# Kernel tuning notes

Measured on AMD Instinct MI355X. Metric: run time of the kernel, lower is better.

## Reference

```python
import jax, jax.numpy as jnp
import numpy as np

SAMPLE_SIZE = 4096  # deterministic mode: first SAMPLE_SIZE flattened pixels
EPS_STD = 1e-8
EPS_PDF = 1e-10


def _std(v):
    # torch.std is unbiased (ddof=1)
    return jnp.std(v, ddof=1)


def _adaptive_sigma(v):
    # sigma=None path: 0.2 * std, clamped to [0.001, 1.0]
    return jnp.clip(_std(v) * 0.2, 0.001, 1.0)


def _normalize(v):
    return (v - jnp.mean(v)) / (_std(v) + EPS_STD)


def _marginal_pdf(values, sigma):
    vn = _normalize(values)                      # [N]
    resid = vn[None, :] - vn[:, None]            # [N, N]
    kernel = jnp.exp(-0.5 * (resid / sigma) ** 2)
    pdf = jnp.mean(kernel, axis=1)               # [N]
    return pdf / (jnp.sum(pdf) + EPS_PDF)


def _joint_pdf(v1, v2, s1, s2):
    vn1 = _normalize(v1)
    vn2 = _normalize(v2)
    r1 = vn1[None, :] - vn1[:, None]             # [N, N]
    r2 = vn2[None, :] - vn2[:, None]             # [N, N]
    kernel = jnp.exp(-0.5 * (r1 / s1) ** 2) * jnp.exp(-0.5 * (r2 / s2) ** 2)
    pdf = jnp.mean(kernel, axis=1)
    return pdf / (jnp.sum(pdf) + EPS_PDF)


def _mi_kde(img1, img2):
    x = img1.reshape(-1)[:SAMPLE_SIZE]
    y = img2.reshape(-1)[:SAMPLE_SIZE]
    s1 = _adaptive_sigma(x)
    s2 = _adaptive_sigma(y)
    p1 = _marginal_pdf(x, s1)
    p2 = _marginal_pdf(y, s2)
    pj = _joint_pdf(x, y, s1, s2)
    ratio = (pj + EPS_PDF) / (p1 * p2 + EPS_PDF)
    log_ratio = jnp.log(jnp.clip(ratio, 1e-10, 1e10))
    return jnp.sum(pj * log_ratio)


def setup_inputs() -> dict:
    key = jax.random.key(0)
    k1, k2, k3 = jax.random.split(key, 3)
    shape = (2, 1, 128, 128)  # [B, C, H, W] images in [0, 1]
    return {
        "fused_img": jax.random.uniform(k1, shape, dtype=jnp.float32),
        "source_img1": jax.random.uniform(k2, shape, dtype=jnp.float32),
        "source_img2": jax.random.uniform(k3, shape, dtype=jnp.float32),
    }


def reference(fused_img, source_img1, source_img2):
    B = fused_img.shape[0]
    total = jnp.float32(0.0)
    for b in range(B):  # small fixed batch loop, matches original
        total = total + _mi_kde(fused_img[b], source_img1[b]) \
                      + _mi_kde(fused_img[b], source_img2[b])
    return -(total / B)
```

## Files before the change

### kernel.cpp

```cpp
#include <hip/hip_runtime.h>

#define N 4096
#define NBIN 1024
#define LOG2E 1.4426950408889634f

__device__ __forceinline__ float fast_exp2(float x) {
#if __has_builtin(__builtin_amdgcn_exp2f)
    return __builtin_amdgcn_exp2f(x);
#else
    return exp2f(x);
#endif
}

__device__ float block_reduce_sum(float v) {
    __shared__ float red[16];
    int lane = threadIdx.x & 63;
    int wid = threadIdx.x >> 6;
    #pragma unroll
    for (int off = 32; off; off >>= 1) v += __shfl_down(v, off, 64);
    if (lane == 0) red[wid] = v;
    __syncthreads();
    if (threadIdx.x == 0) {
        int nw = (int)(blockDim.x >> 6);
        float s = red[0];
        for (int w = 1; w < nw; ++w) s += red[w];
        red[0] = s;
    }
    __syncthreads();
    float r = red[0];
    __syncthreads();
    return r;
}

__device__ float4 block_reduce_stats(float s, float sq, float mn, float mx) {
    __shared__ float4 red4[16];
    int lane = threadIdx.x & 63;
    int wid = threadIdx.x >> 6;
    #pragma unroll
    for (int off = 32; off; off >>= 1) {
        s  += __shfl_down(s, off, 64);
        sq += __shfl_down(sq, off, 64);
        mn  = fminf(mn, __shfl_down(mn, off, 64));
        mx  = fmaxf(mx, __shfl_down(mx, off, 64));
    }
    if (lane == 0) red4[wid] = make_float4(s, sq, mn, mx);
    __syncthreads();
    if (threadIdx.x == 0) {
        float4 r = red4[0];
        #pragma unroll
        for (int w = 1; w < 16; ++w) {
            float4 q = red4[w];
            r.x += q.x; r.y += q.y;
            r.z = fminf(r.z, q.z); r.w = fmaxf(r.w, q.w);
        }
        red4[0] = r;
    }
    __syncthreads();
    float4 r = red4[0];
    __syncthreads();
    return r;
}

__global__ void __launch_bounds__(1024)
k_prep(const float* __restrict__ fused,
       const float* __restrict__ s1,
       const float* __restrict__ s2,
       float2* __restrict__ xa,
       float2* __restrict__ ma,
       float* __restrict__ par,
       float* __restrict__ hcnt,
       float* __restrict__ hmu,
       unsigned int* __restrict__ counter) {
    __shared__ unsigned int cnt[NBIN];
    __shared__ int qs[NBIN];
    int vec = blockIdx.x;
    int b = vec / 3, k = vec % 3;
    const float* src = (k == 0 ? fused : (k == 1 ? s1 : s2)) + b * 16384;
    int tid = threadIdx.x;

    if (vec == 0 && tid == 0) *counter = 0u;
    cnt[tid] = 0u; qs[tid] = 0;

    float v[4];
    float s = 0.f, sq = 0.f, mn = 1e30f, mx = -1e30f;
    #pragma unroll
    for (int t = 0; t < 4; ++t) {
        v[t] = src[tid + t * 1024];
        s += v[t]; sq = fmaf(v[t], v[t], sq);
        mn = fminf(mn, v[t]); mx = fmaxf(mx, v[t]);
    }
    float4 r = block_reduce_stats(s, sq, mn, mx);
    float mean = r.x * (1.0f / 4096.0f);
    float tssq = r.y - 4096.0f * mean * mean;
    float stdv = sqrtf(fmaxf(tssq, 0.f) / 4095.0f);
    float sigma = fminf(fmaxf(0.2f * stdv, 0.001f), 1.0f);
    float inv = 1.0f / (stdv + 1e-8f);
    float c1 = -0.5f * LOG2E / (sigma * sigma);
    float xmin = (r.z - mean) * inv;
    float xmax = (r.w - mean) * inv;
    float range = fmaxf(xmax - xmin, 1e-6f);
    float inv_bw = (float)NBIN / range;
    float binw = range * (1.0f / NBIN);

    float2* xav = xa + (size_t)vec * N;
    float2* mav = ma + (size_t)vec * N;
    __syncthreads();
    #pragma unroll
    for (int t = 0; t < 4; ++t) {
        int i = tid + t * 1024;
        float x = (v[t] - mean) * inv;
        float a = c1 * x * x;
        xav[i] = make_float2(x, a);
        mav[i] = make_float2(-2.0f * c1 * x, a);
        float rel = x - xmin;
        int bb = min(NBIN - 1, max(0, (int)(rel * inv_bw)));
        atomicAdd(&cnt[bb], 1u);
        atomicAdd(&qs[bb], (int)rintf(rel * 16384.0f));
    }
    __syncthreads();
    {
        unsigned int c = cnt[tid];
        hcnt[vec * NBIN + tid] = (float)c;
        float mu = c ? xmin + ((float)qs[tid] / (float)c) * (1.0f / 16384.0f)
                     : xmin + (tid + 0.5f) * binw;
        hmu[vec * NBIN + tid] = mu;
    }
    if (tid == 0) {
        par[vec * 8 + 0] = xmin;
        par[vec * 8 + 1] = inv_bw;
        par[vec * 8 + 2] = binw;
        par[vec * 8 + 3] = c1;
    }
}

__global__ void __launch_bounds__(256, 8)
k_main(const float2* __restrict__ xa,
       const float2* __restrict__ ma,
       const float* __restrict__ par,
       const float* __restrict__ hcnt,
       const float* __restrict__ hmu,
       float* __restrict__ marg,
       float* __restrict__ msum_part,
       float* __restrict__ part, int js) {
    __shared__ float4 sj[128];
    __shared__ float shc[NBIN];
    __shared__ float shm[NBIN];
    const int nib = 4;
    int bid = blockIdx.x;
    int tid = threadIdx.x;

    if (bid < 96) {
        int vec = bid >> 4, ic = bid & 15;
        int i = ic * 256 + tid;
        const float* P = par + vec * 8;
        float xmin = P[0], inv_bw = P[1], c1 = P[3];
        const float* hc = hcnt + vec * NBIN;
        const float* hm = hmu + vec * NBIN;
        #pragma unroll
        for (int u = 0; u < 4; ++u) {
            shc[tid + u * 256] = hc[tid + u * 256];
            shm[tid + u * 256] = hm[tid + u * 256];
        }
        __syncthreads();
        float xi = xa[(size_t)vec * N + i].x;
        float R = sqrtf(45.0f / fabsf(c1));
        int b0 = max(0, (int)((xi - R - xmin) * inv_bw));
        int b1 = min(NBIN - 1, (int)((xi + R - xmin) * inv_bw) + 1);
        float acc = 0.f;
        #pragma unroll 4
        for (int bb = b0; bb <= b1; ++bb) {
            float d = xi - shm[bb];
            acc += shc[bb] * fast_exp2(c1 * d * d);
        }
        float raw = acc * (1.0f / N);
        marg[(size_t)vec * N + i] = raw;
        float tot = block_reduce_sum(raw);
        if (tid == 0) msum_part[bid] = tot;
        return;
    }

    int bid2 = bid - 96;
    int tt = bid2 / (nib * js);
    int rem = bid2 % (nib * js);
    int ib = rem / js, jsp = rem % js;
    int b = tt >> 1, pr = tt & 1;
    int vx = b * 3, vy = b * 3 + 1 + pr;
    int jlen = N / js;
    int j0 = jsp * jlen;
    int ibase = ib * 1024 + tid;

    const float2* xav = xa + (size_t)vx * N;
    const float2* yav = xa + (size_t)vy * N;
    const float2* mxv = ma + (size_t)vx * N;
    const float2* myv = ma + (size_t)vy * N;

    float mx[4], my[4], C[4];
    #pragma unroll
    for (int u = 0; u < 4; ++u) {
        float2 qx = mxv[ibase + u * 256];
        float2 qy = myv[ibase + u * 256];
        mx[u] = qx.x; my[u] = qy.x; C[u] = qx.y + qy.y;
    }
    float acc[4] = {0.f, 0.f, 0.f, 0.f};

    for (int jt = 0; jt < jlen; jt += 128) {
        int cnt = min(128, jlen - jt);
        __syncthreads();
        if (tid < cnt) {
            float2 xq = xav[j0 + jt + tid];
            float2 yq = yav[j0 + jt + tid];
            sj[tid] = make_float4(xq.x, yq.x, xq.y + yq.y, 0.f);
        }
        __syncthreads();
        #pragma unroll 2
        for (int j = 0; j < cnt; j += 2) {
            float4 q0 = sj[j];
            float4 q1 = sj[j + 1];
            float e0[4], e1[4], f0[4], f1[4];
            #pragma unroll
            for (int u = 0; u < 4; ++u) {
                e0[u] = fmaf(my[u], q0.y, fmaf(mx[u], q0.x, C[u])) + q0.z;
                e1[u] = fmaf(my[u], q1.y, fmaf(mx[u], q1.x, C[u])) + q1.z;
            }
            #pragma unroll
            for (int u = 0; u < 4; ++u) {
                f0[u] = fast_exp2(e0[u]);
                f1[u] = fast_exp2(e1[u]);
            }
            #pragma unroll
            for (int u = 0; u < 4; ++u)
                acc[u] += (f0[u] + f1[u]);
        }
    }
    float* dst = part + ((size_t)tt * js + jsp) * N + ibase;
    dst[0]   = acc[0];
    dst[256] = acc[1];
    dst[512] = acc[2];
    dst[768] = acc[3];
}

__global__ void k_redfin(const float* __restrict__ part,
                         const float* __restrict__ marg,
                         const float* __restrict__ msum_part,
                         float* __restrict__ A_part,
                         float* __restrict__ jsum_part,
                         unsigned int* __restrict__ counter,
                         float* __restrict__ out, int js) {
    __shared__ bool isLast;
    __shared__ float svec[6], stask[4], sA[4];
    int blk = blockIdx.x;
    int tt = blk >> 4;
    int ic = blk & 15;
    int b = tt >> 1, pr = tt & 1;
    int vx = b * 3, vy = b * 3 + 1 + pr;
    int i = ic * 256 + threadIdx.x;
    float s = 0.f;
    #pragma unroll 4
    for (int q = 0; q < js; ++q) s += part[((size_t)tt * js + q) * N + i];
    s *= (1.0f / N);
    float rx = marg[(size_t)vx * N + i];
    float ry = marg[(size_t)vy * N + i];
    float a = s * __logf(s / (rx * ry));
    float stot = block_reduce_sum(s);
    float atot = block_reduce_sum(a);
    if (threadIdx.x == 0) {
        jsum_part[blk] = stot;
        A_part[blk] = atot;
        __threadfence();
        unsigned int done = atomicAdd(counter, 1u);
        isLast = (done == 63u);
    }
    __syncthreads();
    if (!isLast) return;
    __threadfence();

    int tid = threadIdx.x;
    if (tid < 6) {
        float ss = 0.f;
        #pragma unroll
        for (int q = 0; q < 16; ++q) ss += msum_part[tid * 16 + q];
        svec[tid] = ss;
    } else if (tid >= 8 && tid < 12) {
        int c = tid - 8;
        float ss = 0.f, aa = 0.f;
        #pragma unroll
        for (int q = 0; q < 16; ++q) {
            ss += jsum_part[c * 16 + q];
            aa += A_part[c * 16 + q];
        }
        stask[c] = ss;
        sA[c] = aa;
    }
    __syncthreads();
    if (tid == 0) {
        float mi = 0.f;
        #pragma unroll
        for (int c = 0; c < 4; ++c) {
            int bb = c >> 1, pp = c & 1;
            int wx = bb * 3, wy = bb * 3 + 1 + pp;
            mi += sA[c] / stask[c] + __logf(svec[wx] * svec[wy] / stask[c]);
        }
        out[0] = -mi * 0.5f;
    }
}

extern "C" void kernel_launch(void* const* d_in, const int* in_sizes, int n_in,
                              void* d_out, int out_size, void* d_ws, size_t ws_size,
                              hipStream_t stream) {
    const float* fused = (const float*)d_in[0];
    const float* s1    = (const float*)d_in[1];
    const float* s2    = (const float*)d_in[2];
    float* out = (float*)d_out;
    float* ws  = (float*)d_ws;

    const size_t off_xa   = 0;
    const size_t off_ma   = off_xa + 12 * (size_t)N;
    const size_t off_par  = off_ma + 12 * (size_t)N;
    const size_t off_hc   = off_par + 64;
    const size_t off_hm   = off_hc + 6 * NBIN;
    const size_t off_mg   = off_hm + 6 * NBIN;
    const size_t off_ms   = off_mg + 6 * (size_t)N;
    const size_t off_A    = off_ms + 128;
    const size_t off_js   = off_A + 64;
    const size_t off_ctr  = off_js + 64;
    const size_t off_part = off_ctr + 16;

    int js = 32;
    while (js > 1 && (off_part + (size_t)4 * js * N) * 4 > ws_size) js >>= 1;

    float2* ws_xa  = (float2*)(ws + off_xa);
    float2* ws_ma  = (float2*)(ws + off_ma);
    float*  ws_par = ws + off_par;
    float*  ws_hc  = ws + off_hc;
    float*  ws_hm  = ws + off_hm;
    float*  ws_mg  = ws + off_mg;
    float*  ws_ms  = ws + off_ms;
    float*  ws_A   = ws + off_A;
    float*  ws_js  = ws + off_js;
    unsigned int* ws_ctr = (unsigned int*)(ws + off_ctr);
    float*  ws_part = ws + off_part;

    k_prep<<<dim3(6), dim3(1024), 0, stream>>>(fused, s1, s2, ws_xa, ws_ma,
                                               ws_par, ws_hc, ws_hm, ws_ctr);
    k_main<<<dim3(96 + 4 * 4 * js), dim3(256), 0, stream>>>(
        ws_xa, ws_ma, ws_par, ws_hc, ws_hm, ws_mg, ws_ms, ws_part, js);
    k_redfin<<<dim3(64), dim3(256), 0, stream>>>(ws_part, ws_mg, ws_ms,
                                                 ws_A, ws_js, ws_ctr, out, js);
}
```

Measured before the change: 35.75 us.

## Fuse final reduction into main kernel via last-block atomic counters

Removes the separate k_redfin launch. The last js-slice block of each (task, i-block) group reduces the partial joint sums and computes the MI terms. It first spin-waits until all 96 marginal blocks have signalled completion, and a final last-block step then writes the output. This saves one kernel launch and its gap, at the cost of extra atomics, a spin-wait that assumes the marginal blocks make progress, and a tail reduction done by only 16 blocks.

```diff
diff --git a/kernel.cpp b/kernel.cpp
--- a/kernel.cpp
+++ b/kernel.cpp
@@ -70,7 +70,7 @@
        float* __restrict__ par,
        float* __restrict__ hcnt,
        float* __restrict__ hmu,
-       unsigned int* __restrict__ counter) {
+       unsigned int* __restrict__ counters) {
     __shared__ unsigned int cnt[NBIN];
     __shared__ int qs[NBIN];
     int vec = blockIdx.x;
@@ -78,7 +78,7 @@
     const float* src = (k == 0 ? fused : (k == 1 ? s1 : s2)) + b * 16384;
     int tid = threadIdx.x;
 
-    if (vec == 0 && tid == 0) *counter = 0u;
+    if (vec == 0 && tid < 32) counters[tid] = 0u;
     cnt[tid] = 0u; qs[tid] = 0;
 
     float v[4];
@@ -141,10 +141,16 @@
        const float* __restrict__ hmu,
        float* __restrict__ marg,
        float* __restrict__ msum_part,
-       float* __restrict__ part, int js) {
+       float* __restrict__ part,
+       float* __restrict__ A_part,
+       float* __restrict__ jsum_part,
+       unsigned int* __restrict__ counters,
+       float* __restrict__ out, int js) {
     __shared__ float4 sj[128];
     __shared__ float shc[NBIN];
     __shared__ float shm[NBIN];
+    __shared__ bool flag;
+    __shared__ float svec[6], stask[4], sA[4];
     const int nib = 4;
     int bid = blockIdx.x;
     int tid = threadIdx.x;
@@ -175,7 +181,11 @@
         float raw = acc * (1.0f / N);
         marg[(size_t)vec * N + i] = raw;
         float tot = block_reduce_sum(raw);
-        if (tid == 0) msum_part[bid] = tot;
+        if (tid == 0) {
+            msum_part[bid] = tot;
+            __threadfence();
+            atomicAdd(&counters[16], 1u);
+        }
         return;
     }
 
@@ -183,6 +193,7 @@
     int tt = bid2 / (nib * js);
     int rem = bid2 % (nib * js);
     int ib = rem / js, jsp = rem % js;
+    int g = tt * nib + ib;
     int b = tt >> 1, pr = tt & 1;
     int vx = b * 3, vy = b * 3 + 1 + pr;
     int jlen = N / js;
@@ -237,44 +248,49 @@
     dst[256] = acc[1];
     dst[512] = acc[2];
     dst[768] = acc[3];
-}
-
-__global__ void k_redfin(const float* __restrict__ part,
-                         const float* __restrict__ marg,
-                         const float* __restrict__ msum_part,
-                         float* __restrict__ A_part,
-                         float* __restrict__ jsum_part,
-                         unsigned int* __restrict__ counter,
-                         float* __restrict__ out, int js) {
-    __shared__ bool isLast;
-    __shared__ float svec[6], stask[4], sA[4];
-    int blk = blockIdx.x;
-    int tt = blk >> 4;
-    int ic = blk & 15;
-    int b = tt >> 1, pr = tt & 1;
-    int vx = b * 3, vy = b * 3 + 1 + pr;
-    int i = ic * 256 + threadIdx.x;
-    float s = 0.f;
-    #pragma unroll 4
-    for (int q = 0; q < js; ++q) s += part[((size_t)tt * js + q) * N + i];
-    s *= (1.0f / N);
-    float rx = marg[(size_t)vx * N + i];
-    float ry = marg[(size_t)vy * N + i];
-    float a = s * __logf(s / (rx * ry));
-    float stot = block_reduce_sum(s);
-    float atot = block_reduce_sum(a);
-    if (threadIdx.x == 0) {
-        jsum_part[blk] = stot;
-        A_part[blk] = atot;
+
+    __syncthreads();
+    if (tid == 0) {
         __threadfence();
-        unsigned int done = atomicAdd(counter, 1u);
-        isLast = (done == 63u);
-    }
-    __syncthreads();
-    if (!isLast) return;
+        unsigned int done = atomicAdd(&counters[g], 1u);
+        flag = (done == (unsigned int)(js - 1));
+    }
+    __syncthreads();
+    if (!flag) return;
+
+    if (tid == 0) {
+        while (__hip_atomic_load(&counters[16], __ATOMIC_ACQUIRE,
+                                 __HIP_MEMORY_SCOPE_AGENT) < 96u) {}
+    }
+    __syncthreads();
     __threadfence();
 
-    int tid = threadIdx.x;
+    float sl = 0.f, al = 0.f;
+    #pragma unroll
+    for (int u = 0; u < 4; ++u) {
+        int i = ibase + u * 256;
+        float s = 0.f;
+        #pragma unroll 4
+        for (int q = 0; q < js; ++q) s += part[((size_t)tt * js + q) * N + i];
+        s *= (1.0f / N);
+        float rx = marg[(size_t)vx * N + i];
+        float ry = marg[(size_t)vy * N + i];
+        sl += s;
+        al += s * __logf(s / (rx * ry));
+    }
+    float stot = block_reduce_sum(sl);
+    float atot = block_reduce_sum(al);
+    if (tid == 0) {
+        jsum_part[g] = stot;
+        A_part[g] = atot;
+        __threadfence();
+        unsigned int done2 = atomicAdd(&counters[17], 1u);
+        flag = (done2 == 15u);
+    }
+    __syncthreads();
+    if (!flag) return;
+    __threadfence();
+
     if (tid < 6) {
         float ss = 0.f;
         #pragma unroll
@@ -284,9 +300,9 @@
         int c = tid - 8;
         float ss = 0.f, aa = 0.f;
         #pragma unroll
-        for (int q = 0; q < 16; ++q) {
-            ss += jsum_part[c * 16 + q];
-            aa += A_part[c * 16 + q];
+        for (int q = 0; q < 4; ++q) {
+            ss += jsum_part[c * 4 + q];
+            aa += A_part[c * 4 + q];
         }
         stask[c] = ss;
         sA[c] = aa;
@@ -321,9 +337,9 @@
     const size_t off_mg   = off_hm + 6 * NBIN;
     const size_t off_ms   = off_mg + 6 * (size_t)N;
     const size_t off_A    = off_ms + 128;
-    const size_t off_js   = off_A + 64;
-    const size_t off_ctr  = off_js + 64;
-    const size_t off_part = off_ctr + 16;
+    const size_t off_js   = off_A + 16;
+    const size_t off_ctr  = off_js + 16;
+    const size_t off_part = off_ctr + 32;
 
     int js = 32;
     while (js > 1 && (off_part + (size_t)4 * js * N) * 4 > ws_size) js >>= 1;
@@ -343,7 +359,6 @@
     k_prep<<<dim3(6), dim3(1024), 0, stream>>>(fused, s1, s2, ws_xa, ws_ma,
                                                ws_par, ws_hc, ws_hm, ws_ctr);
     k_main<<<dim3(96 + 4 * 4 * js), dim3(256), 0, stream>>>(
-        ws_xa, ws_ma, ws_par, ws_hc, ws_hm, ws_mg, ws_ms, ws_part, js);
-    k_redfin<<<dim3(64), dim3(256), 0, stream>>>(ws_part, ws_mg, ws_ms,
-                                                 ws_A, ws_js, ws_ctr, out, js);
-}
+        ws_xa, ws_ma, ws_par, ws_hc, ws_hm, ws_mg, ws_ms, ws_part,
+        ws_A, ws_js, ws_ctr, out, js);
+}
```

Result: slower. 62.10 us (+73.7%).
